# Performance work log

Hardware: AMD Instinct MI355X
Metric: run time of the kernel (lower is better)

Reference implementation:

```python
import jax, jax.numpy as jnp
import numpy as np

NUM_LEVELS = 16
BASE_RES = 16
MAX_RES = 2048
TABLE_SIZE = 1 << 19
FEATS = 2
GROWTH = np.exp((np.log(MAX_RES) - np.log(BASE_RES)) / (NUM_LEVELS - 1))
SCALINGS = jnp.asarray(np.floor(BASE_RES * GROWTH ** np.arange(NUM_LEVELS)), dtype=jnp.float32)  # [L]
OFFSETS = jnp.arange(NUM_LEVELS, dtype=jnp.int32) * TABLE_SIZE  # per-level slice offset into table
AABB_MIN, AABB_MAX = -1.0, 1.0
P1, P2 = jnp.uint32(2654435761), jnp.uint32(805459861)
MASK = jnp.uint32(TABLE_SIZE - 1)


def sh16(d):
    # spherical harmonics components, levels=4 -> 16 components (nerfstudio convention)
    x, y, z = d[..., 0], d[..., 1], d[..., 2]
    xx, yy, zz = x * x, y * y, z * z
    return jnp.stack([
        jnp.full_like(x, 0.28209479177387814),
        -0.48860251190291987 * y,
        0.48860251190291987 * z,
        -0.48860251190291987 * x,
        1.0925484305920792 * x * y,
        -1.0925484305920792 * y * z,
        0.94617469575755997 * zz - 0.31539156525251999,
        -1.0925484305920792 * x * z,
        0.54627421529603959 * (xx - yy),
        0.59004358992664352 * y * (3.0 * xx - yy),
        2.8906114426405538 * x * y * z,
        0.45704579946446572 * y * (5.0 * zz - 1.0),
        0.37317633259011546 * z * (5.0 * zz - 3.0),
        0.45704579946446572 * x * (5.0 * zz - 1.0),
        1.4453057213202769 * z * (xx - yy),
        0.59004358992664352 * x * (xx - 3.0 * yy),
    ], axis=-1)


def hash_fn(x, y, z):
    # spatial hash with wraparound uint32 arithmetic; lower 19 bits match int64 math mod 2^19
    v = x ^ (y * P1) ^ (z * P2)
    return (v & MASK).astype(jnp.int32) + OFFSETS  # [N, L]


def hash_encode(pts, table):
    # pts: [N,3] in [0,1]; table: [L*T, F]
    scaled = pts[:, None, :] * SCALINGS[None, :, None]  # [N, L, 3]
    f = jnp.floor(scaled)
    c = jnp.ceil(scaled)
    off = scaled - f  # [N, L, 3]
    fi = f.astype(jnp.uint32)
    ci = c.astype(jnp.uint32)
    cx, cy, cz = ci[..., 0], ci[..., 1], ci[..., 2]
    fx, fy, fz = fi[..., 0], fi[..., 1], fi[..., 2]
    # corner order matches nerfstudio hashed_0..7
    idx = jnp.stack([
        hash_fn(cx, cy, cz), hash_fn(cx, fy, cz), hash_fn(fx, fy, cz), hash_fn(fx, cy, cz),
        hash_fn(cx, cy, fz), hash_fn(cx, fy, fz), hash_fn(fx, fy, fz), hash_fn(fx, cy, fz),
    ], axis=0)  # [8, N, L]
    feats = table[idx]  # [8, N, L, F]
    ox, oy, oz = off[..., 0:1], off[..., 1:2], off[..., 2:3]
    f03 = feats[0] * ox + feats[3] * (1.0 - ox)
    f12 = feats[1] * ox + feats[2] * (1.0 - ox)
    f56 = feats[5] * ox + feats[6] * (1.0 - ox)
    f47 = feats[4] * ox + feats[7] * (1.0 - ox)
    f0312 = f03 * oy + f12 * (1.0 - oy)
    f4756 = f47 * oy + f56 * (1.0 - oy)
    enc = f0312 * oz + f4756 * (1.0 - oz)  # [N, L, F]
    return enc.reshape(enc.shape[0], NUM_LEVELS * FEATS)


def setup_inputs() -> dict:
    key = jax.random.key(0)
    ks = jax.random.split(key, 16)
    B, S = 4096, 48
    positions = jax.random.uniform(ks[0], (B, S, 3), jnp.float32) * 2.0 - 1.0
    densities = jax.random.normal(ks[1], (B, S, 1), jnp.float32)
    normals = jax.random.normal(ks[2], (B, 3), jnp.float32)
    camera_to_worlds = jax.random.normal(ks[3], (B, 3, 4), jnp.float32) * 0.3
    hash_table = (jax.random.uniform(ks[4], (NUM_LEVELS * TABLE_SIZE, FEATS), jnp.float32) * 2.0 - 1.0) * 1e-4
    def lin(k, i, o):
        return jax.random.normal(k, (i, o), jnp.float32) * (1.0 / np.sqrt(i))
    return {
        'positions': positions, 'densities': densities, 'normals': normals,
        'camera_to_worlds': camera_to_worlds, 'hash_table': hash_table,
        'w1': lin(ks[5], 32, 64), 'b1': jnp.zeros((64,), jnp.float32),
        'w2': lin(ks[6], 64, 16), 'b2': jnp.zeros((16,), jnp.float32),
        'h1': lin(ks[7], 32, 64), 'hb1': jnp.zeros((64,), jnp.float32),
        'h2': lin(ks[8], 64, 64), 'hb2': jnp.zeros((64,), jnp.float32),
        'h3': lin(ks[9], 64, 3), 'hb3': jnp.zeros((3,), jnp.float32),
    }


def reference(positions, densities, normals, camera_to_worlds, hash_table,
              w1, b1, w2, b2, h1, hb1, h2, hb2, h3, hb3):
    B, S, _ = positions.shape
    R = camera_to_worlds[..., :3, :3]
    t = camera_to_worlds[..., :3, 3]
    Rinv = jnp.swapaxes(R, -1, -2)  # pose inverse for rigid transform
    tinv = -jnp.einsum('bij,bj->bi', Rinv, t)
    pos = jnp.einsum('bij,bsj->bsi', Rinv, positions) + tinv[:, None, :]  # world -> camera
    pos = (pos - AABB_MIN) / (AABB_MAX - AABB_MIN)  # SceneBox.get_normalized_positions
    n_cam = jnp.einsum('bij,bj->bi', Rinv, normals)
    n_cam = (n_cam + 1.0) / 2.0  # get_normalized_directions
    d = sh16(n_cam)  # [B, 16]
    d = jnp.broadcast_to(d[:, None, :], (B, S, 16)).reshape(-1, 16)
    selector = jnp.all((pos > 0.0) & (pos < 1.0), axis=-1)
    pos = pos * selector[..., None]
    enc = hash_encode(pos.reshape(-1, 3), hash_table)  # [B*S, 32]
    geo = jax.nn.relu(jax.nn.relu(enc @ w1 + b1) @ w2 + b2)  # mlp_base, out ReLU
    h = jnp.concatenate([d, geo], axis=-1)  # [B*S, 32]
    rgb = jax.nn.sigmoid(jax.nn.relu(jax.nn.relu(h @ h1 + hb1) @ h2 + hb2) @ h3 + hb3)
    rgb = rgb.reshape(B, S, 3)
    weight = jax.nn.softmax(densities, axis=-2)  # softmax over samples
    return jnp.sum(weight * rgb, axis=-2)  # [B, 3] == FieldHeadNames.RGB_AFFINE
```

## Files before the change

kernel.cpp:

```cpp
#include <hip/hip_runtime.h>
#include <math.h>
#include <stdint.h>

#define NLEV 16
#define TSIZE (1u << 19)
#define NB 4096
#define NS 48
#define NPTS (NB * NS)
#define CHUNKS (NPTS / 256)

typedef __attribute__((ext_vector_type(8))) short short8;
typedef __attribute__((ext_vector_type(4))) float f32x4;

struct Scales { float s[NLEV]; };

__device__ __forceinline__ uint32_t hash3(uint32_t x, uint32_t y, uint32_t z) {
    return (x ^ (y * 2654435761u) ^ (z * 805459861u)) & (TSIZE - 1u);
}

__device__ __forceinline__ float sigmoidf(float v) {
    return 1.0f / (1.0f + expf(-v));
}

__device__ __forceinline__ ushort f2b(float f) {
    union { float f; uint32_t u; } v; v.f = f;
    uint32_t r = (v.u + 0x7FFFu + ((v.u >> 16) & 1u)) >> 16;
    return (ushort)r;
}

__device__ __forceinline__ uint32_t pk_relu2(float a, float b) {
    a = fmaxf(a, 0.0f);
    b = fmaxf(b, 0.0f);
    return ((uint32_t)f2b(b) << 16) | (uint32_t)f2b(a);
}

__device__ __forceinline__ uint2 pack4_relu(f32x4 c, f32x4 bias) {
    uint2 o;
    o.x = pk_relu2(c[0] + bias[0], c[1] + bias[1]);
    o.y = pk_relu2(c[2] + bias[2], c[3] + bias[3]);
    return o;
}

#define LDS_FENCE() asm volatile("s_waitcnt lgkmcnt(0)" ::: "memory")

#define MFMA16(a, b, c) __builtin_amdgcn_mfma_f32_16x16x32_bf16((a), (b), (c), 0, 0, 0)

__global__ __launch_bounds__(256) void encode_kernel(
    const float* __restrict__ positions,
    const float* __restrict__ c2w,
    const float* __restrict__ table,
    const float* __restrict__ w1, const float* __restrict__ w2,
    const float* __restrict__ h1, const float* __restrict__ h2,
    const float* __restrict__ h3,
    uint32_t* __restrict__ enc_ws,
    ushort* __restrict__ bank,
    Scales sc)
{
    const int bid = blockIdx.x;
    if (bid == CHUNKS * NLEV) {
        for (int idx = threadIdx.x; idx < 20 * 512; idx += 256) {
            const int f    = idx >> 9;
            const int r    = idx & 511;
            const int lane = r >> 3;
            const int j    = r & 7;
            const int l15  = lane & 15;
            const int quad = lane >> 4;
            const int k8   = quad * 8 + j;
            float val;
            if (f < 4) {
                val = w1[k8 * 64 + f * 16 + l15];
            } else if (f < 6) {
                val = w2[((f - 4) * 32 + k8) * 16 + l15];
            } else if (f < 10) {
                val = h1[k8 * 64 + (f - 6) * 16 + l15];
            } else if (f < 18) {
                const int t = f - 10, nt = t >> 1, kk = t & 1;
                val = h2[(kk * 32 + k8) * 64 + nt * 16 + l15];
            } else {
                val = (l15 < 3) ? h3[((f - 18) * 32 + k8) * 3 + l15] : 0.0f;
            }
            bank[idx] = f2b(val);
        }
        return;
    }

    const int half  = CHUNKS * 8;
    const int ph    = (bid >= half) ? 1 : 0;
    const int q     = bid - ph * half;
    const int x     = q & 7;
    const int l     = x + 8 * ((x & 1) ^ ph);
    const int p     = (q >> 3) * 256 + threadIdx.x;
    const int b     = p / NS;

    const float* M = c2w + b * 12;
    const float px = positions[3 * p + 0];
    const float py = positions[3 * p + 1];
    const float pz = positions[3 * p + 2];
    const float dx = px - M[3], dy = py - M[7], dz = pz - M[11];
    float qx = M[0] * dx + M[4] * dy + M[8] * dz;
    float qy = M[1] * dx + M[5] * dy + M[9] * dz;
    float qz = M[2] * dx + M[6] * dy + M[10] * dz;
    qx = (qx + 1.0f) * 0.5f;
    qy = (qy + 1.0f) * 0.5f;
    qz = (qz + 1.0f) * 0.5f;
    const bool sel = (qx > 0.0f) && (qx < 1.0f) &&
                     (qy > 0.0f) && (qy < 1.0f) &&
                     (qz > 0.0f) && (qz < 1.0f);
    if (!sel) { qx = 0.0f; qy = 0.0f; qz = 0.0f; }

    const float s = sc.s[l];
    const float sx = qx * s, sy = qy * s, sz = qz * s;
    const float fx = floorf(sx), fy = floorf(sy), fz = floorf(sz);
    const float cx = ceilf(sx),  cy = ceilf(sy),  cz = ceilf(sz);
    const float ox = sx - fx, oy = sy - fy, oz = sz - fz;
    const uint32_t fxi = (uint32_t)fx, fyi = (uint32_t)fy, fzi = (uint32_t)fz;
    const uint32_t cxi = (uint32_t)cx, cyi = (uint32_t)cy, czi = (uint32_t)cz;

    const float2* tab = (const float2*)table + (uint32_t)l * TSIZE;
    const float2 g0 = tab[hash3(cxi, cyi, czi)];
    const float2 g1 = tab[hash3(cxi, fyi, czi)];
    const float2 g2 = tab[hash3(fxi, fyi, czi)];
    const float2 g3 = tab[hash3(fxi, cyi, czi)];
    const float2 g4 = tab[hash3(cxi, cyi, fzi)];
    const float2 g5 = tab[hash3(cxi, fyi, fzi)];
    const float2 g6 = tab[hash3(fxi, fyi, fzi)];
    const float2 g7 = tab[hash3(fxi, cyi, fzi)];

    const float omx = 1.0f - ox, omy = 1.0f - oy, omz = 1.0f - oz;
    float f03x = g0.x * ox + g3.x * omx, f03y = g0.y * ox + g3.y * omx;
    float f12x = g1.x * ox + g2.x * omx, f12y = g1.y * ox + g2.y * omx;
    float f56x = g5.x * ox + g6.x * omx, f56y = g5.y * ox + g6.y * omx;
    float f47x = g4.x * ox + g7.x * omx, f47y = g4.y * ox + g7.y * omx;
    float ax = f03x * oy + f12x * omy, ay = f03y * oy + f12y * omy;
    float bx = f47x * oy + f56x * omy, by = f47y * oy + f56y * omy;
    const float ex = ax * oz + bx * omz;
    const float ey = ay * oz + by * omz;
    enc_ws[l * NPTS + p] = ((uint32_t)f2b(ey) << 16) | (uint32_t)f2b(ex);
}

__global__ __launch_bounds__(64) void tail_kernel(
    const uint32_t* __restrict__ enc_ws,
    const float* __restrict__ densities,
    const float* __restrict__ normals,
    const float* __restrict__ c2w,
    const ushort* __restrict__ bank,
    const float* __restrict__ b1, const float* __restrict__ b2,
    const float* __restrict__ hb1, const float* __restrict__ hb2,
    const float* __restrict__ hb3,
    float* __restrict__ out)
{
    __shared__ ushort bufA[48 * 72];
    __shared__ ushort bufB[48 * 72];
    __shared__ ushort bufC[48 * 40];

    const int bidb = blockIdx.x;
    const int p0   = bidb * NS;
    const int lane = threadIdx.x;
    const int l15  = lane & 15;
    const int quad = lane >> 4;

    union XU { uint32_t u[4]; short8 s; };
    XU xu[3];
#pragma unroll
    for (int t = 0; t < 3; ++t)
#pragma unroll
        for (int jj = 0; jj < 4; ++jj)
            xu[t].u[jj] = enc_ws[(quad * 4 + jj) * NPTS + p0 + 16 * t + l15];

    {
        const float* M = c2w + bidb * 12;
        const float n0 = normals[3 * bidb + 0];
        const float n1 = normals[3 * bidb + 1];
        const float n2 = normals[3 * bidb + 2];
        float x = M[0] * n0 + M[4] * n1 + M[8] * n2;
        float y = M[1] * n0 + M[5] * n1 + M[9] * n2;
        float z = M[2] * n0 + M[6] * n1 + M[10] * n2;
        x = (x + 1.0f) * 0.5f;
        y = (y + 1.0f) * 0.5f;
        z = (z + 1.0f) * 0.5f;
        const float xx = x * x, yy = y * y, zz = z * z;
        float v = 0.28209479177387814f;
        v = (l15 == 1)  ? -0.48860251190291987f * y : v;
        v = (l15 == 2)  ?  0.48860251190291987f * z : v;
        v = (l15 == 3)  ? -0.48860251190291987f * x : v;
        v = (l15 == 4)  ?  1.0925484305920792f * x * y : v;
        v = (l15 == 5)  ? -1.0925484305920792f * y * z : v;
        v = (l15 == 6)  ?  0.94617469575756f * zz - 0.31539156525252f : v;
        v = (l15 == 7)  ? -1.0925484305920792f * x * z : v;
        v = (l15 == 8)  ?  0.5462742152960396f * (xx - yy) : v;
        v = (l15 == 9)  ?  0.5900435899266435f * y * (3.0f * xx - yy) : v;
        v = (l15 == 10) ?  2.890611442640554f * x * y * z : v;
        v = (l15 == 11) ?  0.4570457994644657f * y * (5.0f * zz - 1.0f) : v;
        v = (l15 == 12) ?  0.37317633259011546f * z * (5.0f * zz - 3.0f) : v;
        v = (l15 == 13) ?  0.4570457994644657f * x * (5.0f * zz - 1.0f) : v;
        v = (l15 == 14) ?  1.445305721320277f * z * (xx - yy) : v;
        v = (l15 == 15) ?  0.5900435899266435f * x * (xx - 3.0f * yy) : v;
        const ushort shb = f2b(v);
#pragma unroll
        for (int i = 0; i < 12; ++i)
            bufC[(i * 4 + quad) * 40 + l15] = shb;
    }

    const ushort* fb = bank + lane * 8;
#define FRAG(f) (*(const short8*)(fb + (f) * 512))

    const f32x4 zero = {0.0f, 0.0f, 0.0f, 0.0f};

    {
        short8 w[4];
#pragma unroll
        for (int nt = 0; nt < 4; ++nt) w[nt] = FRAG(nt);
        f32x4 c[3][4];
        __builtin_amdgcn_s_setprio(1);
#pragma unroll
        for (int t = 0; t < 3; ++t)
#pragma unroll
            for (int nt = 0; nt < 4; ++nt) c[t][nt] = MFMA16(w[nt], xu[t].s, zero);
        __builtin_amdgcn_s_setprio(0);
        f32x4 b1q[4];
#pragma unroll
        for (int nt = 0; nt < 4; ++nt) b1q[nt] = *(const f32x4*)&b1[nt * 16 + quad * 4];
#pragma unroll
        for (int t = 0; t < 3; ++t)
#pragma unroll
            for (int nt = 0; nt < 4; ++nt)
                *(uint2*)&bufB[(16 * t + l15) * 72 + nt * 16 + quad * 4] =
                    pack4_relu(c[t][nt], b1q[nt]);
    }
    LDS_FENCE();

    {
        const short8 w0 = FRAG(4), w1f = FRAG(5);
        const f32x4 b2q = *(const f32x4*)&b2[quad * 4];
        f32x4 c[3];
        __builtin_amdgcn_s_setprio(1);
#pragma unroll
        for (int t = 0; t < 3; ++t) {
            const short8 a0 = *(const short8*)&bufB[(16 * t + l15) * 72 + quad * 8];
            const short8 a1 = *(const short8*)&bufB[(16 * t + l15) * 72 + 32 + quad * 8];
            c[t] = MFMA16(w0, a0, zero);
            c[t] = MFMA16(w1f, a1, c[t]);
        }
        __builtin_amdgcn_s_setprio(0);
#pragma unroll
        for (int t = 0; t < 3; ++t)
            *(uint2*)&bufC[(16 * t + l15) * 40 + 16 + quad * 4] = pack4_relu(c[t], b2q);
    }
    LDS_FENCE();

    {
        short8 w[4];
#pragma unroll
        for (int nt = 0; nt < 4; ++nt) w[nt] = FRAG(6 + nt);
        f32x4 c[3][4];
        __builtin_amdgcn_s_setprio(1);
#pragma unroll
        for (int t = 0; t < 3; ++t) {
            const short8 a = *(const short8*)&bufC[(16 * t + l15) * 40 + quad * 8];
#pragma unroll
            for (int nt = 0; nt < 4; ++nt) c[t][nt] = MFMA16(w[nt], a, zero);
        }
        __builtin_amdgcn_s_setprio(0);
        f32x4 hb1q[4];
#pragma unroll
        for (int nt = 0; nt < 4; ++nt) hb1q[nt] = *(const f32x4*)&hb1[nt * 16 + quad * 4];
#pragma unroll
        for (int t = 0; t < 3; ++t)
#pragma unroll
            for (int nt = 0; nt < 4; ++nt)
                *(uint2*)&bufA[(16 * t + l15) * 72 + nt * 16 + quad * 4] =
                    pack4_relu(c[t][nt], hb1q[nt]);
    }
    LDS_FENCE();

    {
        short8 w[8];
#pragma unroll
        for (int f = 0; f < 8; ++f) w[f] = FRAG(10 + f);
        f32x4 c[3][4];
        __builtin_amdgcn_s_setprio(1);
#pragma unroll
        for (int t = 0; t < 3; ++t) {
            const short8 a0 = *(const short8*)&bufA[(16 * t + l15) * 72 + quad * 8];
            const short8 a1 = *(const short8*)&bufA[(16 * t + l15) * 72 + 32 + quad * 8];
#pragma unroll
            for (int nt = 0; nt < 4; ++nt) {
                f32x4 u = MFMA16(w[nt * 2], a0, zero);
                c[t][nt] = MFMA16(w[nt * 2 + 1], a1, u);
            }
        }
        __builtin_amdgcn_s_setprio(0);
        f32x4 hb2q[4];
#pragma unroll
        for (int nt = 0; nt < 4; ++nt) hb2q[nt] = *(const f32x4*)&hb2[nt * 16 + quad * 4];
#pragma unroll
        for (int t = 0; t < 3; ++t)
#pragma unroll
            for (int nt = 0; nt < 4; ++nt)
                *(uint2*)&bufB[(16 * t + l15) * 72 + nt * 16 + quad * 4] =
                    pack4_relu(c[t][nt], hb2q[nt]);
    }
    LDS_FENCE();

    f32x4 c5[3];
    {
        const short8 w0 = FRAG(18), w1f = FRAG(19);
        __builtin_amdgcn_s_setprio(1);
#pragma unroll
        for (int t = 0; t < 3; ++t) {
            const short8 a0 = *(const short8*)&bufB[(16 * t + l15) * 72 + quad * 8];
            const short8 a1 = *(const short8*)&bufB[(16 * t + l15) * 72 + 32 + quad * 8];
            c5[t] = MFMA16(w0, a0, zero);
            c5[t] = MFMA16(w1f, a1, c5[t]);
        }
        __builtin_amdgcn_s_setprio(0);
    }
#undef FRAG

    const float d = (lane < NS) ? densities[p0 + lane] : -INFINITY;
    float m = d;
#pragma unroll
    for (int off = 32; off > 0; off >>= 1) m = fmaxf(m, __shfl_xor(m, off));
    const float e = expf(d - m);
    float sum = e;
#pragma unroll
    for (int off = 32; off > 0; off >>= 1) sum += __shfl_xor(sum, off);
    const float wgt = e / sum;
    float wt[3];
#pragma unroll
    for (int t = 0; t < 3; ++t) wt[t] = __shfl(wgt, 16 * t + l15);

    const float h30 = hb3[0], h31 = hb3[1], h32 = hb3[2];
    float a0 = 0.0f, a1 = 0.0f, a2 = 0.0f;
#pragma unroll
    for (int t = 0; t < 3; ++t) {
        a0 += wt[t] * sigmoidf(c5[t][0] + h30);
        a1 += wt[t] * sigmoidf(c5[t][1] + h31);
        a2 += wt[t] * sigmoidf(c5[t][2] + h32);
    }
#pragma unroll
    for (int off = 1; off < 16; off <<= 1) {
        a0 += __shfl_xor(a0, off);
        a1 += __shfl_xor(a1, off);
        a2 += __shfl_xor(a2, off);
    }
    if (lane == 0) {
        out[bidb * 3 + 0] = a0;
        out[bidb * 3 + 1] = a1;
        out[bidb * 3 + 2] = a2;
    }
}

extern "C" void kernel_launch(void* const* d_in, const int* in_sizes, int n_in,
                              void* d_out, int out_size, void* d_ws, size_t ws_size,
                              hipStream_t stream) {
    const float* positions = (const float*)d_in[0];
    const float* densities = (const float*)d_in[1];
    const float* normals   = (const float*)d_in[2];
    const float* c2w       = (const float*)d_in[3];
    const float* table     = (const float*)d_in[4];
    const float* w1  = (const float*)d_in[5];
    const float* b1  = (const float*)d_in[6];
    const float* w2  = (const float*)d_in[7];
    const float* b2  = (const float*)d_in[8];
    const float* h1  = (const float*)d_in[9];
    const float* hb1 = (const float*)d_in[10];
    const float* h2  = (const float*)d_in[11];
    const float* hb2 = (const float*)d_in[12];
    const float* h3  = (const float*)d_in[13];
    const float* hb3 = (const float*)d_in[14];
    float* out = (float*)d_out;

    ushort*   bank   = (ushort*)d_ws;
    uint32_t* enc_ws = (uint32_t*)((char*)d_ws + 20 * 1024);

    Scales sc;
    const double growth = exp((log(2048.0) - log(16.0)) / 15.0);
    for (int i = 0; i < NLEV; ++i)
        sc.s[i] = (float)floor(16.0 * pow(growth, (double)i));

    const int enc_blocks = CHUNKS * NLEV + 1;
    encode_kernel<<<enc_blocks, 256, 0, stream>>>(
        positions, c2w, table, w1, w2, h1, h2, h3, enc_ws, bank, sc);
    tail_kernel<<<NB, 64, 0, stream>>>(
        enc_ws, densities, normals, c2w, bank, b1, b2, hb1, hb2, hb3, out);
}
```

Baseline: 203.2 us.

## Fuse hash encoding into the MLP tail kernel and drop the encoding workspace

The separate encode kernel and its global workspace round trip are removed. Each 64-thread block now computes the encoding for its own 48 samples, with every lane handling 4 levels for 3 sample slots, and feeds the result straight into the MFMA operand registers. The weight bank packing moves into its own one-block kernel. This saves the write and re-read of the encoded features and one large launch. In exchange, the random table gathers now run in small blocks with 12 independent gather sets per lane, which may hurt latency hiding and level-wise cache locality.

New measurement: 287.3 us. +41.4%, slower.

```diff
diff --git a/kernel.cpp b/kernel.cpp
--- a/kernel.cpp
+++ b/kernel.cpp
@@ -7,7 +7,6 @@
 #define NB 4096
 #define NS 48
 #define NPTS (NB * NS)
-#define CHUNKS (NPTS / 256)
 
 typedef __attribute__((ext_vector_type(8))) short short8;
 typedef __attribute__((ext_vector_type(4))) float f32x4;
@@ -45,109 +44,48 @@
 
 #define MFMA16(a, b, c) __builtin_amdgcn_mfma_f32_16x16x32_bf16((a), (b), (c), 0, 0, 0)
 
-__global__ __launch_bounds__(256) void encode_kernel(
-    const float* __restrict__ positions,
-    const float* __restrict__ c2w,
-    const float* __restrict__ table,
+__global__ __launch_bounds__(256) void bank_kernel(
     const float* __restrict__ w1, const float* __restrict__ w2,
     const float* __restrict__ h1, const float* __restrict__ h2,
-    const float* __restrict__ h3,
-    uint32_t* __restrict__ enc_ws,
-    ushort* __restrict__ bank,
-    Scales sc)
+    const float* __restrict__ h3, ushort* __restrict__ bank)
 {
-    const int bid = blockIdx.x;
-    if (bid == CHUNKS * NLEV) {
-        for (int idx = threadIdx.x; idx < 20 * 512; idx += 256) {
-            const int f    = idx >> 9;
-            const int r    = idx & 511;
-            const int lane = r >> 3;
-            const int j    = r & 7;
-            const int l15  = lane & 15;
-            const int quad = lane >> 4;
-            const int k8   = quad * 8 + j;
-            float val;
-            if (f < 4) {
-                val = w1[k8 * 64 + f * 16 + l15];
-            } else if (f < 6) {
-                val = w2[((f - 4) * 32 + k8) * 16 + l15];
-            } else if (f < 10) {
-                val = h1[k8 * 64 + (f - 6) * 16 + l15];
-            } else if (f < 18) {
-                const int t = f - 10, nt = t >> 1, kk = t & 1;
-                val = h2[(kk * 32 + k8) * 64 + nt * 16 + l15];
-            } else {
-                val = (l15 < 3) ? h3[((f - 18) * 32 + k8) * 3 + l15] : 0.0f;
-            }
-            bank[idx] = f2b(val);
-        }
-        return;
-    }
-
-    const int half  = CHUNKS * 8;
-    const int ph    = (bid >= half) ? 1 : 0;
-    const int q     = bid - ph * half;
-    const int x     = q & 7;
-    const int l     = x + 8 * ((x & 1) ^ ph);
-    const int p     = (q >> 3) * 256 + threadIdx.x;
-    const int b     = p / NS;
-
-    const float* M = c2w + b * 12;
-    const float px = positions[3 * p + 0];
-    const float py = positions[3 * p + 1];
-    const float pz = positions[3 * p + 2];
-    const float dx = px - M[3], dy = py - M[7], dz = pz - M[11];
-    float qx = M[0] * dx + M[4] * dy + M[8] * dz;
-    float qy = M[1] * dx + M[5] * dy + M[9] * dz;
-    float qz = M[2] * dx + M[6] * dy + M[10] * dz;
-    qx = (qx + 1.0f) * 0.5f;
-    qy = (qy + 1.0f) * 0.5f;
-    qz = (qz + 1.0f) * 0.5f;
-    const bool sel = (qx > 0.0f) && (qx < 1.0f) &&
-                     (qy > 0.0f) && (qy < 1.0f) &&
-                     (qz > 0.0f) && (qz < 1.0f);
-    if (!sel) { qx = 0.0f; qy = 0.0f; qz = 0.0f; }
-
-    const float s = sc.s[l];
-    const float sx = qx * s, sy = qy * s, sz = qz * s;
-    const float fx = floorf(sx), fy = floorf(sy), fz = floorf(sz);
-    const float cx = ceilf(sx),  cy = ceilf(sy),  cz = ceilf(sz);
-    const float ox = sx - fx, oy = sy - fy, oz = sz - fz;
-    const uint32_t fxi = (uint32_t)fx, fyi = (uint32_t)fy, fzi = (uint32_t)fz;
-    const uint32_t cxi = (uint32_t)cx, cyi = (uint32_t)cy, czi = (uint32_t)cz;
-
-    const float2* tab = (const float2*)table + (uint32_t)l * TSIZE;
-    const float2 g0 = tab[hash3(cxi, cyi, czi)];
-    const float2 g1 = tab[hash3(cxi, fyi, czi)];
-    const float2 g2 = tab[hash3(fxi, fyi, czi)];
-    const float2 g3 = tab[hash3(fxi, cyi, czi)];
-    const float2 g4 = tab[hash3(cxi, cyi, fzi)];
-    const float2 g5 = tab[hash3(cxi, fyi, fzi)];
-    const float2 g6 = tab[hash3(fxi, fyi, fzi)];
-    const float2 g7 = tab[hash3(fxi, cyi, fzi)];
-
-    const float omx = 1.0f - ox, omy = 1.0f - oy, omz = 1.0f - oz;
-    float f03x = g0.x * ox + g3.x * omx, f03y = g0.y * ox + g3.y * omx;
-    float f12x = g1.x * ox + g2.x * omx, f12y = g1.y * ox + g2.y * omx;
-    float f56x = g5.x * ox + g6.x * omx, f56y = g5.y * ox + g6.y * omx;
-    float f47x = g4.x * ox + g7.x * omx, f47y = g4.y * ox + g7.y * omx;
-    float ax = f03x * oy + f12x * omy, ay = f03y * oy + f12y * omy;
-    float bx = f47x * oy + f56x * omy, by = f47y * oy + f56y * omy;
-    const float ex = ax * oz + bx * omz;
-    const float ey = ay * oz + by * omz;
-    enc_ws[l * NPTS + p] = ((uint32_t)f2b(ey) << 16) | (uint32_t)f2b(ex);
-}
-
-__global__ __launch_bounds__(64) void tail_kernel(
-    const uint32_t* __restrict__ enc_ws,
+    for (int idx = threadIdx.x; idx < 20 * 512; idx += 256) {
+        const int f    = idx >> 9;
+        const int r    = idx & 511;
+        const int lane = r >> 3;
+        const int j    = r & 7;
+        const int l15  = lane & 15;
+        const int quad = lane >> 4;
+        const int k8   = quad * 8 + j;
+        float val;
+        if (f < 4) {
+            val = w1[k8 * 64 + f * 16 + l15];
+        } else if (f < 6) {
+            val = w2[((f - 4) * 32 + k8) * 16 + l15];
+        } else if (f < 10) {
+            val = h1[k8 * 64 + (f - 6) * 16 + l15];
+        } else if (f < 18) {
+            const int t = f - 10, nt = t >> 1, kk = t & 1;
+            val = h2[(kk * 32 + k8) * 64 + nt * 16 + l15];
+        } else {
+            val = (l15 < 3) ? h3[((f - 18) * 32 + k8) * 3 + l15] : 0.0f;
+        }
+        bank[idx] = f2b(val);
+    }
+}
+
+__global__ __launch_bounds__(64) void fused_kernel(
+    const float* __restrict__ positions,
     const float* __restrict__ densities,
     const float* __restrict__ normals,
     const float* __restrict__ c2w,
+    const float* __restrict__ table,
     const ushort* __restrict__ bank,
     const float* __restrict__ b1, const float* __restrict__ b2,
     const float* __restrict__ hb1, const float* __restrict__ hb2,
     const float* __restrict__ hb3,
-    float* __restrict__ out)
+    float* __restrict__ out,
+    Scales sc)
 {
     __shared__ ushort bufA[48 * 72];
     __shared__ ushort bufB[48 * 72];
@@ -159,16 +97,77 @@
     const int l15  = lane & 15;
     const int quad = lane >> 4;
 
+    float sq[4];
+#pragma unroll
+    for (int jj = 0; jj < 4; ++jj) {
+        float v = sc.s[jj];
+        v = (quad == 1) ? sc.s[4 + jj]  : v;
+        v = (quad == 2) ? sc.s[8 + jj]  : v;
+        v = (quad == 3) ? sc.s[12 + jj] : v;
+        sq[jj] = v;
+    }
+
+    const float* M = c2w + bidb * 12;
+    float qx[3], qy[3], qz[3];
+#pragma unroll
+    for (int t = 0; t < 3; ++t) {
+        const int p = p0 + 16 * t + l15;
+        const float px = positions[3 * p + 0];
+        const float py = positions[3 * p + 1];
+        const float pz = positions[3 * p + 2];
+        const float dx = px - M[3], dy = py - M[7], dz = pz - M[11];
+        float x = M[0] * dx + M[4] * dy + M[8] * dz;
+        float y = M[1] * dx + M[5] * dy + M[9] * dz;
+        float z = M[2] * dx + M[6] * dy + M[10] * dz;
+        x = (x + 1.0f) * 0.5f;
+        y = (y + 1.0f) * 0.5f;
+        z = (z + 1.0f) * 0.5f;
+        const bool sel = (x > 0.0f) && (x < 1.0f) &&
+                         (y > 0.0f) && (y < 1.0f) &&
+                         (z > 0.0f) && (z < 1.0f);
+        qx[t] = sel ? x : 0.0f;
+        qy[t] = sel ? y : 0.0f;
+        qz[t] = sel ? z : 0.0f;
+    }
+
     union XU { uint32_t u[4]; short8 s; };
     XU xu[3];
 #pragma unroll
-    for (int t = 0; t < 3; ++t)
-#pragma unroll
-        for (int jj = 0; jj < 4; ++jj)
-            xu[t].u[jj] = enc_ws[(quad * 4 + jj) * NPTS + p0 + 16 * t + l15];
-
-    {
-        const float* M = c2w + bidb * 12;
+    for (int t = 0; t < 3; ++t) {
+#pragma unroll
+        for (int jj = 0; jj < 4; ++jj) {
+            const float s  = sq[jj];
+            const float sx = qx[t] * s, sy = qy[t] * s, sz = qz[t] * s;
+            const float fx = floorf(sx), fy = floorf(sy), fz = floorf(sz);
+            const float cx = ceilf(sx),  cy = ceilf(sy),  cz = ceilf(sz);
+            const float ox = sx - fx, oy = sy - fy, oz = sz - fz;
+            const uint32_t fxi = (uint32_t)fx, fyi = (uint32_t)fy, fzi = (uint32_t)fz;
+            const uint32_t cxi = (uint32_t)cx, cyi = (uint32_t)cy, czi = (uint32_t)cz;
+
+            const float2* tab = (const float2*)table + (uint32_t)(quad * 4 + jj) * TSIZE;
+            const float2 g0 = tab[hash3(cxi, cyi, czi)];
+            const float2 g1 = tab[hash3(cxi, fyi, czi)];
+            const float2 g2 = tab[hash3(fxi, fyi, czi)];
+            const float2 g3 = tab[hash3(fxi, cyi, czi)];
+            const float2 g4 = tab[hash3(cxi, cyi, fzi)];
+            const float2 g5 = tab[hash3(cxi, fyi, fzi)];
+            const float2 g6 = tab[hash3(fxi, fyi, fzi)];
+            const float2 g7 = tab[hash3(fxi, cyi, fzi)];
+
+            const float omx = 1.0f - ox, omy = 1.0f - oy, omz = 1.0f - oz;
+            float f03x = g0.x * ox + g3.x * omx, f03y = g0.y * ox + g3.y * omx;
+            float f12x = g1.x * ox + g2.x * omx, f12y = g1.y * ox + g2.y * omx;
+            float f56x = g5.x * ox + g6.x * omx, f56y = g5.y * ox + g6.y * omx;
+            float f47x = g4.x * ox + g7.x * omx, f47y = g4.y * ox + g7.y * omx;
+            float ax = f03x * oy + f12x * omy, ay = f03y * oy + f12y * omy;
+            float bx = f47x * oy + f56x * omy, by = f47y * oy + f56y * omy;
+            const float ex = ax * oz + bx * omz;
+            const float ey = ay * oz + by * omz;
+            xu[t].u[jj] = ((uint32_t)f2b(ey) << 16) | (uint32_t)f2b(ex);
+        }
+    }
+
+    {
         const float n0 = normals[3 * bidb + 0];
         const float n1 = normals[3 * bidb + 1];
         const float n2 = normals[3 * bidb + 2];
@@ -371,17 +370,15 @@
     const float* hb3 = (const float*)d_in[14];
     float* out = (float*)d_out;
 
-    ushort*   bank   = (ushort*)d_ws;
-    uint32_t* enc_ws = (uint32_t*)((char*)d_ws + 20 * 1024);
+    ushort* bank = (ushort*)d_ws;
 
     Scales sc;
     const double growth = exp((log(2048.0) - log(16.0)) / 15.0);
     for (int i = 0; i < NLEV; ++i)
         sc.s[i] = (float)floor(16.0 * pow(growth, (double)i));
 
-    const int enc_blocks = CHUNKS * NLEV + 1;
-    encode_kernel<<<enc_blocks, 256, 0, stream>>>(
-        positions, c2w, table, w1, w2, h1, h2, h3, enc_ws, bank, sc);
-    tail_kernel<<<NB, 64, 0, stream>>>(
-        enc_ws, densities, normals, c2w, bank, b1, b2, hb1, hb2, hb3, out);
-}
+    bank_kernel<<<1, 256, 0, stream>>>(w1, w2, h1, h2, h3, bank);
+    fused_kernel<<<NB, 64, 0, stream>>>(
+        positions, densities, normals, c2w, table, bank,
+        b1, b2, hb1, hb2, hb3, out, sc);
+}
```

## Pass MLP activations between layers via cross-lane shuffles instead of LDS

Applied to the files above, without the earlier changes.

The tail kernel no longer stages inter-layer activations in shared memory. MFMA outputs are packed to bf16 in registers and redistributed into the next layer's operand layout with __shfl. The tail kernel also now packs four 64-lane waves (one ray each) per 256-thread block, and the softmax over densities moves ahead of the MLP. This removes LDS stores, loads and fences and the per-block LDS footprint. In exchange it adds many ds_bpermute shuffles and select instructions and raises register pressure.

Result: no change. 199.8 us (-1.6%).

```diff
diff --git a/kernel.cpp b/kernel.cpp
--- a/kernel.cpp
+++ b/kernel.cpp
@@ -33,15 +33,6 @@
     b = fmaxf(b, 0.0f);
     return ((uint32_t)f2b(b) << 16) | (uint32_t)f2b(a);
 }
-
-__device__ __forceinline__ uint2 pack4_relu(f32x4 c, f32x4 bias) {
-    uint2 o;
-    o.x = pk_relu2(c[0] + bias[0], c[1] + bias[1]);
-    o.y = pk_relu2(c[2] + bias[2], c[3] + bias[3]);
-    return o;
-}
-
-#define LDS_FENCE() asm volatile("s_waitcnt lgkmcnt(0)" ::: "memory")
 
 #define MFMA16(a, b, c) __builtin_amdgcn_mfma_f32_16x16x32_bf16((a), (b), (c), 0, 0, 0)
 
@@ -138,7 +129,7 @@
     enc_ws[l * NPTS + p] = ((uint32_t)f2b(ey) << 16) | (uint32_t)f2b(ex);
 }
 
-__global__ __launch_bounds__(64) void tail_kernel(
+__global__ __launch_bounds__(256) void tail_kernel(
     const uint32_t* __restrict__ enc_ws,
     const float* __restrict__ densities,
     const float* __restrict__ normals,
@@ -149,17 +140,15 @@
     const float* __restrict__ hb3,
     float* __restrict__ out)
 {
-    __shared__ ushort bufA[48 * 72];
-    __shared__ ushort bufB[48 * 72];
-    __shared__ ushort bufC[48 * 40];
-
-    const int bidb = blockIdx.x;
+    const int bidb = blockIdx.x * 4 + (threadIdx.x >> 6);
     const int p0   = bidb * NS;
-    const int lane = threadIdx.x;
+    const int lane = threadIdx.x & 63;
     const int l15  = lane & 15;
     const int quad = lane >> 4;
+    const int hiq  = quad >> 1;
 
     union XU { uint32_t u[4]; short8 s; };
+
     XU xu[3];
 #pragma unroll
     for (int t = 0; t < 3; ++t)
@@ -167,8 +156,22 @@
         for (int jj = 0; jj < 4; ++jj)
             xu[t].u[jj] = enc_ws[(quad * 4 + jj) * NPTS + p0 + 16 * t + l15];
 
-    {
-        const float* M = c2w + bidb * 12;
+    const float d = (lane < NS) ? densities[p0 + lane] : -INFINITY;
+    float m = d;
+#pragma unroll
+    for (int off = 32; off > 0; off >>= 1) m = fmaxf(m, __shfl_xor(m, off));
+    const float e = expf(d - m);
+    float sum = e;
+#pragma unroll
+    for (int off = 32; off > 0; off >>= 1) sum += __shfl_xor(sum, off);
+    const float wgt = e / sum;
+    float wt[3];
+#pragma unroll
+    for (int t = 0; t < 3; ++t) wt[t] = __shfl(wgt, 16 * t + l15);
+
+    const float* M = c2w + bidb * 12;
+    float shv;
+    {
         const float n0 = normals[3 * bidb + 0];
         const float n1 = normals[3 * bidb + 1];
         const float n2 = normals[3 * bidb + 2];
@@ -195,140 +198,151 @@
         v = (l15 == 13) ?  0.4570457994644657f * x * (5.0f * zz - 1.0f) : v;
         v = (l15 == 14) ?  1.445305721320277f * z * (xx - yy) : v;
         v = (l15 == 15) ?  0.5900435899266435f * x * (xx - 3.0f * yy) : v;
-        const ushort shb = f2b(v);
-#pragma unroll
-        for (int i = 0; i < 12; ++i)
-            bufC[(i * 4 + quad) * 40 + l15] = shb;
+        shv = v;
+    }
+    uint32_t shw[8];
+#pragma unroll
+    for (int i = 0; i < 8; ++i) {
+        const float s0 = __shfl(shv, 2 * i);
+        const float s1 = __shfl(shv, 2 * i + 1);
+        shw[i] = ((uint32_t)f2b(s1) << 16) | (uint32_t)f2b(s0);
     }
 
     const ushort* fb = bank + lane * 8;
 #define FRAG(f) (*(const short8*)(fb + (f) * 512))
 
     const f32x4 zero = {0.0f, 0.0f, 0.0f, 0.0f};
+    const int srcq = 2 * (quad & 1);
+
+    uint32_t pw[3][4][2];
 
     {
         short8 w[4];
 #pragma unroll
         for (int nt = 0; nt < 4; ++nt) w[nt] = FRAG(nt);
-        f32x4 c[3][4];
+        f32x4 b1q[4];
+#pragma unroll
+        for (int nt = 0; nt < 4; ++nt) b1q[nt] = *(const f32x4*)&b1[nt * 16 + quad * 4];
         __builtin_amdgcn_s_setprio(1);
 #pragma unroll
-        for (int t = 0; t < 3; ++t)
-#pragma unroll
-            for (int nt = 0; nt < 4; ++nt) c[t][nt] = MFMA16(w[nt], xu[t].s, zero);
+        for (int t = 0; t < 3; ++t) {
+#pragma unroll
+            for (int nt = 0; nt < 4; ++nt) {
+                const f32x4 c = MFMA16(w[nt], xu[t].s, zero);
+                pw[t][nt][0] = pk_relu2(c[0] + b1q[nt][0], c[1] + b1q[nt][1]);
+                pw[t][nt][1] = pk_relu2(c[2] + b1q[nt][2], c[3] + b1q[nt][3]);
+            }
+        }
         __builtin_amdgcn_s_setprio(0);
-        f32x4 b1q[4];
-#pragma unroll
-        for (int nt = 0; nt < 4; ++nt) b1q[nt] = *(const f32x4*)&b1[nt * 16 + quad * 4];
-#pragma unroll
-        for (int t = 0; t < 3; ++t)
-#pragma unroll
-            for (int nt = 0; nt < 4; ++nt)
-                *(uint2*)&bufB[(16 * t + l15) * 72 + nt * 16 + quad * 4] =
-                    pack4_relu(c[t][nt], b1q[nt]);
-    }
-    LDS_FENCE();
-
+    }
+
+    uint32_t pg[3][2];
     {
         const short8 w0 = FRAG(4), w1f = FRAG(5);
         const f32x4 b2q = *(const f32x4*)&b2[quad * 4];
-        f32x4 c[3];
-        __builtin_amdgcn_s_setprio(1);
 #pragma unroll
         for (int t = 0; t < 3; ++t) {
-            const short8 a0 = *(const short8*)&bufB[(16 * t + l15) * 72 + quad * 8];
-            const short8 a1 = *(const short8*)&bufB[(16 * t + l15) * 72 + 32 + quad * 8];
-            c[t] = MFMA16(w0, a0, zero);
-            c[t] = MFMA16(w1f, a1, c[t]);
-        }
-        __builtin_amdgcn_s_setprio(0);
-#pragma unroll
-        for (int t = 0; t < 3; ++t)
-            *(uint2*)&bufC[(16 * t + l15) * 40 + 16 + quad * 4] = pack4_relu(c[t], b2q);
-    }
-    LDS_FENCE();
+            XU a0u, a1u;
+#pragma unroll
+            for (int jj = 0; jj < 4; ++jj) {
+                const int src = 16 * (srcq + (jj >> 1)) + l15;
+                const uint32_t v0 = __shfl(pw[t][0][jj & 1], src);
+                const uint32_t v1 = __shfl(pw[t][1][jj & 1], src);
+                const uint32_t v2 = __shfl(pw[t][2][jj & 1], src);
+                const uint32_t v3 = __shfl(pw[t][3][jj & 1], src);
+                a0u.u[jj] = hiq ? v1 : v0;
+                a1u.u[jj] = hiq ? v3 : v2;
+            }
+            f32x4 c = MFMA16(w0, a0u.s, zero);
+            c = MFMA16(w1f, a1u.s, c);
+            pg[t][0] = pk_relu2(c[0] + b2q[0], c[1] + b2q[1]);
+            pg[t][1] = pk_relu2(c[2] + b2q[2], c[3] + b2q[3]);
+        }
+    }
 
     {
         short8 w[4];
 #pragma unroll
         for (int nt = 0; nt < 4; ++nt) w[nt] = FRAG(6 + nt);
-        f32x4 c[3][4];
-        __builtin_amdgcn_s_setprio(1);
+        f32x4 hb1q[4];
+#pragma unroll
+        for (int nt = 0; nt < 4; ++nt) hb1q[nt] = *(const f32x4*)&hb1[nt * 16 + quad * 4];
 #pragma unroll
         for (int t = 0; t < 3; ++t) {
-            const short8 a = *(const short8*)&bufC[(16 * t + l15) * 40 + quad * 8];
-#pragma unroll
-            for (int nt = 0; nt < 4; ++nt) c[t][nt] = MFMA16(w[nt], a, zero);
-        }
-        __builtin_amdgcn_s_setprio(0);
-        f32x4 hb1q[4];
-#pragma unroll
-        for (int nt = 0; nt < 4; ++nt) hb1q[nt] = *(const f32x4*)&hb1[nt * 16 + quad * 4];
-#pragma unroll
-        for (int t = 0; t < 3; ++t)
-#pragma unroll
-            for (int nt = 0; nt < 4; ++nt)
-                *(uint2*)&bufA[(16 * t + l15) * 72 + nt * 16 + quad * 4] =
-                    pack4_relu(c[t][nt], hb1q[nt]);
-    }
-    LDS_FENCE();
+            XU au;
+#pragma unroll
+            for (int jj = 0; jj < 4; ++jj) {
+                const int src = 16 * (srcq + (jj >> 1)) + l15;
+                const uint32_t g = __shfl(pg[t][jj & 1], src);
+                const uint32_t s_lo = shw[jj];
+                const uint32_t s_hi = shw[4 + jj];
+                const uint32_t sh_sel = (quad & 1) ? s_hi : s_lo;
+                au.u[jj] = (quad >= 2) ? g : sh_sel;
+            }
+            __builtin_amdgcn_s_setprio(1);
+#pragma unroll
+            for (int nt = 0; nt < 4; ++nt) {
+                const f32x4 c = MFMA16(w[nt], au.s, zero);
+                pw[t][nt][0] = pk_relu2(c[0] + hb1q[nt][0], c[1] + hb1q[nt][1]);
+                pw[t][nt][1] = pk_relu2(c[2] + hb1q[nt][2], c[3] + hb1q[nt][3]);
+            }
+            __builtin_amdgcn_s_setprio(0);
+        }
+    }
 
     {
         short8 w[8];
 #pragma unroll
         for (int f = 0; f < 8; ++f) w[f] = FRAG(10 + f);
-        f32x4 c[3][4];
-        __builtin_amdgcn_s_setprio(1);
+        f32x4 hb2q[4];
+#pragma unroll
+        for (int nt = 0; nt < 4; ++nt) hb2q[nt] = *(const f32x4*)&hb2[nt * 16 + quad * 4];
 #pragma unroll
         for (int t = 0; t < 3; ++t) {
-            const short8 a0 = *(const short8*)&bufA[(16 * t + l15) * 72 + quad * 8];
-            const short8 a1 = *(const short8*)&bufA[(16 * t + l15) * 72 + 32 + quad * 8];
+            XU a0u, a1u;
+#pragma unroll
+            for (int jj = 0; jj < 4; ++jj) {
+                const int src = 16 * (srcq + (jj >> 1)) + l15;
+                const uint32_t v0 = __shfl(pw[t][0][jj & 1], src);
+                const uint32_t v1 = __shfl(pw[t][1][jj & 1], src);
+                const uint32_t v2 = __shfl(pw[t][2][jj & 1], src);
+                const uint32_t v3 = __shfl(pw[t][3][jj & 1], src);
+                a0u.u[jj] = hiq ? v1 : v0;
+                a1u.u[jj] = hiq ? v3 : v2;
+            }
+            __builtin_amdgcn_s_setprio(1);
 #pragma unroll
             for (int nt = 0; nt < 4; ++nt) {
-                f32x4 u = MFMA16(w[nt * 2], a0, zero);
-                c[t][nt] = MFMA16(w[nt * 2 + 1], a1, u);
-            }
-        }
-        __builtin_amdgcn_s_setprio(0);
-        f32x4 hb2q[4];
-#pragma unroll
-        for (int nt = 0; nt < 4; ++nt) hb2q[nt] = *(const f32x4*)&hb2[nt * 16 + quad * 4];
-#pragma unroll
-        for (int t = 0; t < 3; ++t)
-#pragma unroll
-            for (int nt = 0; nt < 4; ++nt)
-                *(uint2*)&bufB[(16 * t + l15) * 72 + nt * 16 + quad * 4] =
-                    pack4_relu(c[t][nt], hb2q[nt]);
-    }
-    LDS_FENCE();
+                f32x4 u = MFMA16(w[nt * 2], a0u.s, zero);
+                const f32x4 c = MFMA16(w[nt * 2 + 1], a1u.s, u);
+                pw[t][nt][0] = pk_relu2(c[0] + hb2q[nt][0], c[1] + hb2q[nt][1]);
+                pw[t][nt][1] = pk_relu2(c[2] + hb2q[nt][2], c[3] + hb2q[nt][3]);
+            }
+            __builtin_amdgcn_s_setprio(0);
+        }
+    }
 
     f32x4 c5[3];
     {
         const short8 w0 = FRAG(18), w1f = FRAG(19);
-        __builtin_amdgcn_s_setprio(1);
 #pragma unroll
         for (int t = 0; t < 3; ++t) {
-            const short8 a0 = *(const short8*)&bufB[(16 * t + l15) * 72 + quad * 8];
-            const short8 a1 = *(const short8*)&bufB[(16 * t + l15) * 72 + 32 + quad * 8];
-            c5[t] = MFMA16(w0, a0, zero);
-            c5[t] = MFMA16(w1f, a1, c5[t]);
-        }
-        __builtin_amdgcn_s_setprio(0);
+            XU a0u, a1u;
+#pragma unroll
+            for (int jj = 0; jj < 4; ++jj) {
+                const int src = 16 * (srcq + (jj >> 1)) + l15;
+                const uint32_t v0 = __shfl(pw[t][0][jj & 1], src);
+                const uint32_t v1 = __shfl(pw[t][1][jj & 1], src);
+                const uint32_t v2 = __shfl(pw[t][2][jj & 1], src);
+                const uint32_t v3 = __shfl(pw[t][3][jj & 1], src);
+                a0u.u[jj] = hiq ? v1 : v0;
+                a1u.u[jj] = hiq ? v3 : v2;
+            }
+            f32x4 c = MFMA16(w0, a0u.s, zero);
+            c5[t] = MFMA16(w1f, a1u.s, c);
+        }
     }
 #undef FRAG
-
-    const float d = (lane < NS) ? densities[p0 + lane] : -INFINITY;
-    float m = d;
-#pragma unroll
-    for (int off = 32; off > 0; off >>= 1) m = fmaxf(m, __shfl_xor(m, off));
-    const float e = expf(d - m);
-    float sum = e;
-#pragma unroll
-    for (int off = 32; off > 0; off >>= 1) sum += __shfl_xor(sum, off);
-    const float wgt = e / sum;
-    float wt[3];
-#pragma unroll
-    for (int t = 0; t < 3; ++t) wt[t] = __shfl(wgt, 16 * t + l15);
 
     const float h30 = hb3[0], h31 = hb3[1], h32 = hb3[2];
     float a0 = 0.0f, a1 = 0.0f, a2 = 0.0f;
@@ -382,6 +396,6 @@
     const int enc_blocks = CHUNKS * NLEV + 1;
     encode_kernel<<<enc_blocks, 256, 0, stream>>>(
         positions, c2w, table, w1, w2, h1, h2, h3, enc_ws, bank, sc);
-    tail_kernel<<<NB, 64, 0, stream>>>(
+    tail_kernel<<<NB / 4, 256, 0, stream>>>(
         enc_ws, densities, normals, c2w, bank, b1, b2, hb1, hb2, hb3, out);
 }
```
